# Kernel optimization log

Hardware: AMD Instinct MI355X
Metric: run time of the kernel (lower is better)

## Reference

```python
import jax, jax.numpy as jnp
import numpy as np

B, L, E, H = 64, 2048, 300, 1  # batch, seq_len, embed_size, lstm hidden_size


def setup_inputs() -> dict:
    key = jax.random.key(0)
    ks = jax.random.split(key, 6)
    x = jax.random.normal(ks[0], (B, L, E), dtype=jnp.float32)
    source_lengths = jax.random.randint(ks[1], (B,), 0, L, dtype=jnp.int32)
    s = 1.0 / np.sqrt(H)  # pytorch LSTM init: U(-1/sqrt(H), 1/sqrt(H))
    W_ih = jax.random.uniform(ks[2], (4 * H, E), minval=-s, maxval=s, dtype=jnp.float32)
    W_hh = jax.random.uniform(ks[3], (4 * H, H), minval=-s, maxval=s, dtype=jnp.float32)
    b_ih = jax.random.uniform(ks[4], (4 * H,), minval=-s, maxval=s, dtype=jnp.float32)
    b_hh = jax.random.uniform(ks[5], (4 * H,), minval=-s, maxval=s, dtype=jnp.float32)
    return {"x": x, "source_lengths": source_lengths, "W_ih": W_ih, "W_hh": W_hh,
            "b_ih": b_ih, "b_hh": b_hh}


def _lstm_scores(x, W_ih, W_hh, b_ih, b_hh):
    # x: [B, L, E] -> hidden states [B, L, H]; pytorch gate order i, f, g, o.
    xg = jnp.einsum('ble,ge->blg', x, W_ih) + (b_ih + b_hh)  # [B, L, 4H]
    Bb = x.shape[0]
    Hh = W_hh.shape[1]
    h0 = jnp.zeros((Bb, Hh), x.dtype)
    c0 = jnp.zeros((Bb, Hh), x.dtype)

    def step(carry, g_t):
        h, c = carry
        gates = g_t + h @ W_hh.T  # [B, 4H]
        i, f, g, o = jnp.split(gates, 4, axis=-1)
        i = jax.nn.sigmoid(i)
        f = jax.nn.sigmoid(f)
        g = jnp.tanh(g)
        o = jax.nn.sigmoid(o)
        c = f * c + i * g
        h = o * jnp.tanh(c)
        return (h, c), h

    _, hs = jax.lax.scan(step, (h0, c0), jnp.swapaxes(xg, 0, 1))  # [L, B, H]
    return jnp.swapaxes(hs, 0, 1)  # [B, L, H]


def reference(x, source_lengths, W_ih, W_hh, b_ih, b_hh):
    hs = _lstm_scores(x, W_ih, W_hh, b_ih, b_hh)  # [B, L, 1]
    scores = hs[..., 0]  # squeeze -> [B, L]
    # Faithful to original (buggy) mask: only timestep 0 is masked to -inf,
    # and only when source_lengths[i] > 0.
    scores = scores.at[:, 0].set(jnp.where(source_lengths > 0, -jnp.inf, scores[:, 0]))
    attn = jax.nn.softmax(scores, axis=1)  # [B, L]
    # diag(attn) @ x == per-timestep broadcast scale
    return attn[:, :, None] * x  # [B, L, E]
```

## Files before the change

kernel.cpp:

```cpp
#include <hip/hip_runtime.h>
#include <math.h>

#define BATCH 64
#define SEQL  2048
#define EMB   300
#define NROWS (BATCH * SEQL)
#define NV4   (NROWS * 75)
#define U     16
#define CHUNK 32
#define WARM  64
#define NCHUNK (SEQL / CHUNK)

typedef float floatx4 __attribute__((ext_vector_type(4)));

static __device__ __forceinline__ float fast_rcp(float x) {
#if __has_builtin(__builtin_amdgcn_rcpf)
    return __builtin_amdgcn_rcpf(x);
#else
    return 1.0f / x;
#endif
}

static __device__ __forceinline__ float fast_exp2(float x) {
#if __has_builtin(__builtin_amdgcn_exp2f)
    return __builtin_amdgcn_exp2f(x);
#else
    return exp2f(x);
#endif
}

__global__ void __launch_bounds__(256) proj_kernel(
    const float* __restrict__ x, const float* __restrict__ Wih,
    const float* __restrict__ bih, const float* __restrict__ bhh,
    float4* __restrict__ xg)
{
    const float L2E = 1.4426950408889634f;
    const int lane = threadIdx.x & 63;
    const int wid  = threadIdx.x >> 6;

    float4 w0[4], w1[4];
    float  bs[4];
#pragma unroll
    for (int k = 0; k < 4; ++k) {
        const float4* wr = (const float4*)(Wih + k * EMB);
        w0[k] = wr[lane];
        w1[k] = (lane < 11) ? wr[64 + lane] : make_float4(0.f, 0.f, 0.f, 0.f);
        bs[k] = bih[k] + bhh[k];
    }

    for (int row = blockIdx.x * 4 + wid; row < NROWS; row += gridDim.x * 4) {
        const float4* xr = (const float4*)(x + (size_t)row * EMB);
        float4 v0 = xr[lane];
        float4 v1 = (lane < 11) ? xr[64 + lane] : make_float4(0.f, 0.f, 0.f, 0.f);
        float acc[4];
#pragma unroll
        for (int k = 0; k < 4; ++k) {
            float a;
            a  = v0.x * w0[k].x; a = fmaf(v0.y, w0[k].y, a);
            a  = fmaf(v0.z, w0[k].z, a); a = fmaf(v0.w, w0[k].w, a);
            a  = fmaf(v1.x, w1[k].x, a); a = fmaf(v1.y, w1[k].y, a);
            a  = fmaf(v1.z, w1[k].z, a); a = fmaf(v1.w, w1[k].w, a);
            acc[k] = a;
        }
#pragma unroll
        for (int m = 32; m >= 1; m >>= 1) {
#pragma unroll
            for (int k = 0; k < 4; ++k) acc[k] += __shfl_xor(acc[k], m, 64);
        }
        if (lane == 0) {
            int t = row & (SEQL - 1);
            int bb = row >> 11;
            float ai = acc[0] + bs[0];
            float af = acc[1] + bs[1];
            float ag = acc[2] + bs[2];
            float ao = acc[3] + bs[3];
            xg[t * BATCH + bb] =
                make_float4(-L2E * ai, -L2E * af, -2.f * L2E * ag, -L2E * ao);
        }
    }
}

__global__ void __launch_bounds__(64) lstm_scan_kernel(
    const float4* __restrict__ xg, const int* __restrict__ slen,
    const float* __restrict__ Whh, float* __restrict__ score,
    float2* __restrict__ part)
{
    const float L2E = 1.4426950408889634f;
    const float K2  = -2.f * L2E;
    const int b = threadIdx.x;
    const int k = blockIdx.x;
    const float wi = -L2E * Whh[0];
    const float wf = -L2E * Whh[1];
    const float wg = K2   * Whh[2];
    const float wo = -L2E * Whh[3];
    const bool masked = slen[b] > 0;

    const int cstart = k * CHUNK;
    const int tstart = (cstart >= WARM) ? (cstart - WARM) : 0;
    const int nch    = (cstart + CHUNK - tstart) / U;

    float h = 0.f, c = 0.f;
    float m = -1e30f, sum = 0.f;

    float4 bufA[U], bufB[U];
#pragma unroll
    for (int u = 0; u < U; ++u) bufA[u] = xg[(tstart + u) * BATCH + b];

#define STEP(g4, T_) do {                                                  \
    float gi = fast_rcp(1.f + fast_exp2(fmaf(h, wi, (g4).x)));             \
    float gf = fast_rcp(1.f + fast_exp2(fmaf(h, wf, (g4).y)));             \
    float go = fast_rcp(1.f + fast_exp2(fmaf(h, wo, (g4).w)));             \
    float gg = fmaf(2.f, fast_rcp(1.f + fast_exp2(fmaf(h, wg, (g4).z))), -1.f); \
    float ig  = gi * gg;                                                   \
    float f2  = K2 * gf;                                                   \
    float ig2 = K2 * ig;                                                   \
    float targ = fmaf(f2, c, ig2);            \
    c = fmaf(gf, c, ig);                                                   \
    float tc = fmaf(2.f, fast_rcp(1.f + fast_exp2(targ)), -1.f);           \
    h = go * tc;                                                           \
    if (do_store) {                                                        \
        score[(T_) * BATCH + b] = h;                                       \
        if (!((T_) == 0 && masked)) {                                      \
            float mn = fmaxf(m, h);                                        \
            sum = fmaf(sum, fast_exp2((m - mn) * L2E),                     \
                       fast_exp2((h - mn) * L2E));                         \
            m = mn;                                                        \
        }                                                                  \
    }                                                                      \
} while (0)

    for (int ich = 0; ich < nch; ich += 2) {
        int tA = tstart + ich * U;
        int tB = tA + U;
#pragma unroll
        for (int u = 0; u < U; ++u)
            bufB[u] = xg[(tB + u) * BATCH + b];
        {
            const bool do_store = (tA >= cstart);
#pragma unroll
            for (int u = 0; u < U; ++u) STEP(bufA[u], tA + u);
        }
        if (ich + 2 < nch) {
#pragma unroll
            for (int u = 0; u < U; ++u)
                bufA[u] = xg[(tB + U + u) * BATCH + b];
        }
        {
            const bool do_store = (tB >= cstart);
#pragma unroll
            for (int u = 0; u < U; ++u) STEP(bufB[u], tB + u);
        }
    }
#undef STEP

    part[b * NCHUNK + k] = make_float2(m, sum);
}

__global__ void __launch_bounds__(64) reduce_kernel(
    const float2* __restrict__ part, float* __restrict__ stats)
{
    const float L2E = 1.4426950408889634f;
    const int b = blockIdx.x;
    const int l = threadIdx.x;

    float2 p = part[b * NCHUNK + l];

    float M = p.x;
#pragma unroll
    for (int s = 32; s >= 1; s >>= 1) M = fmaxf(M, __shfl_xor(M, s, 64));

    float sum = p.y * fast_exp2((p.x - M) * L2E);
#pragma unroll
    for (int s = 32; s >= 1; s >>= 1) sum += __shfl_xor(sum, s, 64);

    if (l == 0) {
        stats[b] = M;
        stats[BATCH + b] = fast_rcp(sum);
    }
}

__global__ void __launch_bounds__(256) scale_kernel(
    const float4* __restrict__ x4, const float* __restrict__ score,
    const float* __restrict__ stats, const int* __restrict__ slen,
    float4* __restrict__ out4)
{
    const float L2E = 1.4426950408889634f;
    const int stride = gridDim.x * blockDim.x;
    for (int idx = blockIdx.x * blockDim.x + threadIdx.x; idx < NV4; idx += stride) {
        unsigned row = (unsigned)idx / 75u;
        unsigned bb = row >> 11;
        unsigned t  = row & 2047u;
        float s = score[t * BATCH + bb];
        float a = fast_exp2((s - stats[bb]) * L2E) * stats[BATCH + bb];
        if (t == 0u && slen[bb] > 0) a = 0.f;
        float4 v = x4[idx];
        floatx4 r = {a * v.x, a * v.y, a * v.z, a * v.w};
        __builtin_nontemporal_store(r, (floatx4*)&out4[idx]);
    }
}

extern "C" void kernel_launch(void* const* d_in, const int* in_sizes, int n_in,
                              void* d_out, int out_size, void* d_ws, size_t ws_size,
                              hipStream_t stream)
{
    const float* x    = (const float*)d_in[0];
    const int*   slen = (const int*)d_in[1];
    const float* Wih  = (const float*)d_in[2];
    const float* Whh  = (const float*)d_in[3];
    const float* bih  = (const float*)d_in[4];
    const float* bhh  = (const float*)d_in[5];
    float* out = (float*)d_out;

    char* ws = (char*)d_ws;
    float4* xg    = (float4*)ws;
    float*  score = (float*)(ws + (size_t)NROWS * 16);
    float*  stats = (float*)(ws + (size_t)NROWS * 20);
    float2* part  = (float2*)(ws + (size_t)NROWS * 20 + 1024);

    proj_kernel<<<4096, 256, 0, stream>>>(x, Wih, bih, bhh, xg);
    lstm_scan_kernel<<<NCHUNK, 64, 0, stream>>>(xg, slen, Whh, score, part);
    reduce_kernel<<<BATCH, 64, 0, stream>>>(part, stats);
    scale_kernel<<<4096, 256, 0, stream>>>((const float4*)x, score, stats, slen,
                                           (float4*)out);
}
```

Before: 100.9 us.

## Halve scan chunk size and fuse softmax reduction into last-finishing scan block

The LSTM scan chunk drops from 32 to 16 timesteps with a 48-step warmup, giving 128 blocks instead of 64. This shortens the serial recurrence each block runs and spreads the scan over more CUs, though each block redoes more warmup steps relative to the steps it keeps. The separate reduce kernel is removed: an atomic ticket lets the last scan block merge the per-chunk softmax partials, saving one launch. Scheduling barriers are added to keep prefetch loads grouped ahead of the compute.

```diff
diff --git a/kernel.cpp b/kernel.cpp
--- a/kernel.cpp
+++ b/kernel.cpp
@@ -6,10 +6,10 @@
 #define EMB   300
 #define NROWS (BATCH * SEQL)
 #define NV4   (NROWS * 75)
-#define U     16
-#define CHUNK 32
-#define WARM  64
-#define NCHUNK (SEQL / CHUNK)
+#define U     8
+#define CHUNK 16
+#define WARM  48
+#define NBLK  (SEQL / CHUNK)
 
 typedef float floatx4 __attribute__((ext_vector_type(4)));
 
@@ -32,8 +32,10 @@
 __global__ void __launch_bounds__(256) proj_kernel(
     const float* __restrict__ x, const float* __restrict__ Wih,
     const float* __restrict__ bih, const float* __restrict__ bhh,
-    float4* __restrict__ xg)
-{
+    float4* __restrict__ xg, unsigned* __restrict__ counter)
+{
+    if (blockIdx.x == 0 && threadIdx.x == 0) *counter = 0u;
+
     const float L2E = 1.4426950408889634f;
     const int lane = threadIdx.x & 63;
     const int wid  = threadIdx.x >> 6;
@@ -70,20 +72,18 @@
         if (lane == 0) {
             int t = row & (SEQL - 1);
             int bb = row >> 11;
-            float ai = acc[0] + bs[0];
-            float af = acc[1] + bs[1];
-            float ag = acc[2] + bs[2];
-            float ao = acc[3] + bs[3];
-            xg[t * BATCH + bb] =
-                make_float4(-L2E * ai, -L2E * af, -2.f * L2E * ag, -L2E * ao);
-        }
-    }
-}
-
-__global__ void __launch_bounds__(64) lstm_scan_kernel(
+            xg[t * BATCH + bb] = make_float4(
+                -L2E * (acc[0] + bs[0]), -L2E * (acc[1] + bs[1]),
+                -2.f * L2E * (acc[2] + bs[2]), -L2E * (acc[3] + bs[3]));
+        }
+    }
+}
+
+__global__ void __launch_bounds__(64, 1) lstm_scan_kernel(
     const float4* __restrict__ xg, const int* __restrict__ slen,
     const float* __restrict__ Whh, float* __restrict__ score,
-    float2* __restrict__ part)
+    float2* __restrict__ part, float* __restrict__ stats,
+    unsigned* __restrict__ counter)
 {
     const float L2E = 1.4426950408889634f;
     const float K2  = -2.f * L2E;
@@ -105,6 +105,7 @@
     float4 bufA[U], bufB[U];
 #pragma unroll
     for (int u = 0; u < U; ++u) bufA[u] = xg[(tstart + u) * BATCH + b];
+    __builtin_amdgcn_sched_barrier(0);
 
 #define STEP(g4, T_) do {                                                  \
     float gi = fast_rcp(1.f + fast_exp2(fmaf(h, wi, (g4).x)));             \
@@ -135,6 +136,7 @@
 #pragma unroll
         for (int u = 0; u < U; ++u)
             bufB[u] = xg[(tB + u) * BATCH + b];
+        __builtin_amdgcn_sched_barrier(0);
         {
             const bool do_store = (tA >= cstart);
 #pragma unroll
@@ -145,6 +147,7 @@
             for (int u = 0; u < U; ++u)
                 bufA[u] = xg[(tB + U + u) * BATCH + b];
         }
+        __builtin_amdgcn_sched_barrier(0);
         {
             const bool do_store = (tB >= cstart);
 #pragma unroll
@@ -153,29 +156,35 @@
     }
 #undef STEP
 
-    part[b * NCHUNK + k] = make_float2(m, sum);
-}
-
-__global__ void __launch_bounds__(64) reduce_kernel(
-    const float2* __restrict__ part, float* __restrict__ stats)
-{
-    const float L2E = 1.4426950408889634f;
-    const int b = blockIdx.x;
-    const int l = threadIdx.x;
-
-    float2 p = part[b * NCHUNK + l];
-
-    float M = p.x;
-#pragma unroll
-    for (int s = 32; s >= 1; s >>= 1) M = fmaxf(M, __shfl_xor(M, s, 64));
-
-    float sum = p.y * fast_exp2((p.x - M) * L2E);
-#pragma unroll
-    for (int s = 32; s >= 1; s >>= 1) sum += __shfl_xor(sum, s, 64);
-
-    if (l == 0) {
-        stats[b] = M;
-        stats[BATCH + b] = fast_rcp(sum);
+    part[b * NBLK + k] = make_float2(m, sum);
+
+    __threadfence();
+    unsigned ticket = 0;
+    if (b == 0) ticket = atomicAdd(counter, 1u);
+    ticket = (unsigned)__shfl((int)ticket, 0, 64);
+    if (ticket == NBLK - 1) {
+        __threadfence();
+        const int l = b;
+        for (int bb = 0; bb < BATCH; ++bb) {
+            float2 p0 = part[bb * NBLK + l];
+            float2 p1 = part[bb * NBLK + 64 + l];
+            float M  = fmaxf(p0.x, p1.x);
+            float s  = fmaf(p0.y, fast_exp2((p0.x - M) * L2E),
+                            p1.y * fast_exp2((p1.x - M) * L2E));
+#pragma unroll
+            for (int sh = 32; sh >= 1; sh >>= 1) {
+                float Mo = __shfl_xor(M, sh, 64);
+                float so = __shfl_xor(s, sh, 64);
+                float Mn = fmaxf(M, Mo);
+                s = fmaf(s, fast_exp2((M - Mn) * L2E),
+                         so * fast_exp2((Mo - Mn) * L2E));
+                M = Mn;
+            }
+            if (l == 0) {
+                stats[bb] = M;
+                stats[BATCH + bb] = fast_rcp(s);
+            }
+        }
     }
 }
 
@@ -212,14 +221,15 @@
     float* out = (float*)d_out;
 
     char* ws = (char*)d_ws;
-    float4* xg    = (float4*)ws;
-    float*  score = (float*)(ws + (size_t)NROWS * 16);
-    float*  stats = (float*)(ws + (size_t)NROWS * 20);
-    float2* part  = (float2*)(ws + (size_t)NROWS * 20 + 1024);
-
-    proj_kernel<<<4096, 256, 0, stream>>>(x, Wih, bih, bhh, xg);
-    lstm_scan_kernel<<<NCHUNK, 64, 0, stream>>>(xg, slen, Whh, score, part);
-    reduce_kernel<<<BATCH, 64, 0, stream>>>(part, stats);
+    float4*   xg      = (float4*)ws;
+    float*    score   = (float*)(ws + (size_t)NROWS * 16);
+    float*    stats   = (float*)(ws + (size_t)NROWS * 20);
+    float2*   part    = (float2*)(ws + (size_t)NROWS * 20 + 1024);
+    unsigned* counter = (unsigned*)(ws + (size_t)NROWS * 20 + 1024 + 65536);
+
+    proj_kernel<<<4096, 256, 0, stream>>>(x, Wih, bih, bhh, xg, counter);
+    lstm_scan_kernel<<<NBLK, 64, 0, stream>>>(xg, slen, Whh, score, part, stats,
+                                              counter);
     scale_kernel<<<4096, 256, 0, stream>>>((const float4*)x, score, stats, slen,
                                            (float4*)out);
 }
```

After: 137.1 us. 1.36x slower.
